# Kernel optimization log

Hardware: AMD Instinct MI355X
Metric: run time of the kernel (lower is better)

The kernel has to match this reference:

```python
import jax, jax.numpy as jnp
import numpy as np
from functools import partial

N_QUBITS = 8
DEPTH = 2
INPUT_DIM = 128
HIDDEN_DIM = N_QUBITS  # required: hx = o * tanh(cx) elementwise
DIM = 2 ** N_QUBITS

# Z expectation matrix: ZMAT[k, i] = +1/-1 depending on bit of basis state k at wire i
# (wire 0 is the most-significant qubit, PennyLane convention)
_bits = ((np.arange(DIM)[:, None] >> (N_QUBITS - 1 - np.arange(N_QUBITS)[None, :])) & 1)
ZMAT = jnp.asarray(1.0 - 2.0 * _bits, dtype=jnp.float32)  # [2**n, n]


def _apply_1q(state, G, wire):
    """Apply 2x2 gate G ([2,2] shared or [B,2,2] batched) on `wire`."""
    B = state.shape[0]
    left, right = 2 ** wire, 2 ** (N_QUBITS - wire - 1)
    s = state.reshape(B, left, 2, right)
    if G.ndim == 2:
        s = jnp.einsum('ij,bljr->blir', G, s)
    else:
        s = jnp.einsum('bij,bljr->blir', G, s)
    return s.reshape(B, DIM)


def _apply_cnot(state, wire):
    """CNOT with control=wire, target=wire+1 (adjacent)."""
    B = state.shape[0]
    left, right = 2 ** wire, 2 ** (N_QUBITS - wire - 2)
    s = state.reshape(B, left, 2, 2, right)
    s = jnp.concatenate([s[:, :, :1], s[:, :, 1:, ::-1]], axis=2)
    return s.reshape(B, DIM)


def quantum_gate(angles, params):
    """angles: [B, n] RX rotation angles; params: [depth, n] RY angles.
    Returns [B, n] PauliZ expectations (exact statevector simulation)."""
    B = angles.shape[0]
    state = jnp.zeros((B, DIM), dtype=jnp.complex64).at[:, 0].set(1.0)
    # RX encoding layer (batched angles)
    c = jnp.cos(angles / 2).astype(jnp.complex64)
    s = (-1j) * jnp.sin(angles / 2).astype(jnp.complex64)
    for i in range(N_QUBITS):
        G = jnp.stack([jnp.stack([c[:, i], s[:, i]], -1),
                       jnp.stack([s[:, i], c[:, i]], -1)], -2)  # [B,2,2]
        state = _apply_1q(state, G, i)
    # variational layers: RY (shared params) + CNOT chain
    cp = jnp.cos(params / 2).astype(jnp.complex64)
    sp = jnp.sin(params / 2).astype(jnp.complex64)
    for d in range(DEPTH):
        for i in range(N_QUBITS):
            G = jnp.array([[1.0, 0.0], [0.0, 1.0]], jnp.complex64)
            G = jnp.stack([jnp.stack([cp[d, i], -sp[d, i]]),
                           jnp.stack([sp[d, i], cp[d, i]])])  # [2,2]
            state = _apply_1q(state, G, i)
        for i in range(N_QUBITS - 1):
            state = _apply_cnot(state, i)
    probs = (state.real ** 2 + state.imag ** 2)  # [B, 2**n]
    return probs @ ZMAT  # [B, n]


def setup_inputs() -> dict:
    key = jax.random.key(0)
    ks = jax.random.split(key, 13)
    T, B = 256, 1024
    cat = INPUT_DIM + HIDDEN_DIM
    lin_scale = 1.0 / np.sqrt(cat)
    d = {'inputs': jax.random.normal(ks[0], (T, B, INPUT_DIM), jnp.float32)}
    for idx, g in enumerate(['f', 'i', 'g', 'o']):
        d[f'W{g}'] = jax.random.uniform(ks[1 + 3 * idx], (N_QUBITS, cat), jnp.float32, -lin_scale, lin_scale)
        d[f'b{g}'] = jax.random.uniform(ks[2 + 3 * idx], (N_QUBITS,), jnp.float32, -lin_scale, lin_scale)
        d[f'P{g}'] = jax.random.normal(ks[3 + 3 * idx], (DEPTH, N_QUBITS), jnp.float32)
    return d


def reference(inputs, Wf, bf, Pf, Wi, bi, Pi, Wg, bg, Pg, Wo, bo, Po):
    T, B, _ = inputs.shape
    h0 = jnp.zeros((B, HIDDEN_DIM), inputs.dtype)
    c0 = jnp.zeros((B, HIDDEN_DIM), inputs.dtype)

    def step(carry, x):
        hx, cx = carry
        comb = jnp.concatenate([x, hx], axis=1)  # [B, input+hidden]
        f = jax.nn.sigmoid(quantum_gate(comb @ Wf.T + bf, Pf))
        i = jax.nn.sigmoid(quantum_gate(comb @ Wi.T + bi, Pi))
        g = jnp.tanh(quantum_gate(comb @ Wg.T + bg, Pg))
        o = jax.nn.sigmoid(quantum_gate(comb @ Wo.T + bo, Po))
        cx = f * cx + i * g
        hx = o * jnp.tanh(cx)
        return (hx, cx), hx

    (hx, cx), outputs = jax.lax.scan(step, (h0, c0), inputs)
    return outputs, (hx, cx)
```

## Files before the change

### kernel.cpp

```cpp
#include <hip/hip_runtime.h>
#include <math.h>

#define TS 256
#define BB 1024
#define NQ 8
#define INDIM 128
#define CATDIM 136
#define INV2PI 0.15915494309189535f
#define LOG2E  1.4426950408889634f
#define CHUNK 32

typedef float v2f __attribute__((ext_vector_type(2)));

__device__ __forceinline__ float dpp_xor1(float v) {
    return __int_as_float(__builtin_amdgcn_mov_dpp(__float_as_int(v), 0xB1, 0xF, 0xF, true));
}
__device__ __forceinline__ float dpp_xor2(float v) {
    return __int_as_float(__builtin_amdgcn_mov_dpp(__float_as_int(v), 0x4E, 0xF, 0xF, true));
}
__device__ __forceinline__ float dpp_xor8(float v) {
    return __int_as_float(__builtin_amdgcn_mov_dpp(__float_as_int(v), 0x128, 0xF, 0xF, true));
}
__device__ __forceinline__ float swz4(float v)  {
    return __int_as_float(__builtin_amdgcn_ds_swizzle(__float_as_int(v), 0x101F));
}
__device__ __forceinline__ float swz16(float v) {
    return __int_as_float(__builtin_amdgcn_ds_swizzle(__float_as_int(v), 0x401F));
}
__device__ __forceinline__ float swz20(float v) {
    return __int_as_float(__builtin_amdgcn_ds_swizzle(__float_as_int(v), 0x501F));
}
__device__ __forceinline__ float hw_sin(float x) { float r; asm("v_sin_f32 %0, %1" : "=v"(r) : "v"(x)); return r; }
__device__ __forceinline__ float hw_cos(float x) { float r; asm("v_cos_f32 %0, %1" : "=v"(r) : "v"(x)); return r; }
__device__ __forceinline__ float hw_exp(float x) { float r; asm("v_exp_f32 %0, %1" : "=v"(r) : "v"(x)); return r; }
__device__ __forceinline__ float hw_rcp(float x) { float r; asm("v_rcp_f32 %0, %1" : "=v"(r) : "v"(x)); return r; }
__device__ __forceinline__ v2f mk2(float x, float y) { v2f r; r.x = x; r.y = y; return r; }
__device__ __forceinline__ v2f pk_fma(v2f a, v2f b, v2f c) {
    v2f d; asm("v_pk_fma_f32 %0, %1, %2, %3" : "=v"(d) : "v"(a), "v"(b), "v"(c)); return d;
}

__launch_bounds__(128, 1)
__global__ void qlstm_pc(const float* __restrict__ x,
    const float* __restrict__ Wf, const float* __restrict__ bf, const float* __restrict__ Pf,
    const float* __restrict__ Wi, const float* __restrict__ bi, const float* __restrict__ Pi,
    const float* __restrict__ Wg, const float* __restrict__ bg, const float* __restrict__ Pg,
    const float* __restrict__ Wo, const float* __restrict__ bo, const float* __restrict__ Po,
    float* __restrict__ out, float* __restrict__ hst, float* __restrict__ cst)
{
    const int tid = threadIdx.x;
    const int wv = tid >> 6;
    const int lane = tid & 63;
    const int b = blockIdx.x;

    __shared__ float xp[TS * 32];

    const float* Wlist[4] = { Wf, Wi, Wg, Wo };
    const float* blist[4] = { bf, bi, bg, bo };
    const float* Plist[4] = { Pf, Pi, Pg, Po };

    const int l0 = lane & 1, l1 = (lane >> 1) & 1, l3 = (lane >> 3) & 1;
    const int q = 4 * l0 + 2 * l1 + l3;
    const int g = ((lane >> 2) & 1) | ((lane >> 3) & 2);

    float Chw[8], nSw[8], hsp0[8], cp0c[8];
    v2f whq[4];
    float sel[8];
    float kl = 0.f, Aa = 0.f, Bb = 0.f;
    if (wv == 1) {
        const float* P = Plist[g];
        #pragma unroll
        for (int w = 0; w < 8; ++w) {
            float s1, c1, s0, c0;
            __sincosf(P[8 + w], &s1, &c1);
            __sincosf(P[w], &s0, &c0);
            Chw[w] = 0.5f * c1;
            nSw[w] = -s1;
            hsp0[w] = 0.5f * s0;
            cp0c[w] = c0;
        }
        const float* Wq = Wlist[g] + q * CATDIM + INDIM;
        #pragma unroll
        for (int p2 = 0; p2 < 4; ++p2)
            whq[p2] = mk2(INV2PI * Wq[q ^ (2 * p2)], INV2PI * Wq[q ^ (2 * p2 + 1)]);
        kl = ((g == 2) ? 2.f : -1.f) * LOG2E;
        Aa = (g == 2) ? 1.f : 0.f;
        Bb = (g == 2) ? -1.f : 1.f;
        #pragma unroll
        for (int i = 0; i < 8; ++i) sel[i] = (q == i) ? kl : 0.f;
    }

    float s0h = 0.f, s1h = 0.f, s2h = 0.f, s3h = 0.f;
    float s4h = 0.f, s5h = 0.f, s6h = 0.f, s7h = 0.f;
    float c_own = 0.f, hv = 0.f;
    const bool emit = (wv == 1) && ((lane & 0x34) == 0);
    float* optr = out + (size_t)b * NQ + q;

    const int pq = lane >> 3;
    const int kg = lane & 7;

    auto fill_chunk = [&](int base) {
        float4 wfrag[4][4];
        float bias_w[4];
        #pragma unroll
        for (int g4 = 0; g4 < 4; ++g4) {
            const float* Wr = Wlist[g4] + pq * CATDIM + kg * 16;
            #pragma unroll
            for (int c4 = 0; c4 < 4; ++c4) {
                float4 v = *(const float4*)(Wr + c4 * 4);
                v.x *= INV2PI; v.y *= INV2PI; v.z *= INV2PI; v.w *= INV2PI;
                wfrag[g4][c4] = v;
            }
            bias_w[g4] = blist[g4][pq] * INV2PI;
        }
        for (int tt = 0; tt < CHUNK; ++tt) {
            const int t = base + tt;
            const float* xr = x + ((size_t)t * BB + b) * INDIM + kg * 16;
            float4 x0 = *(const float4*)(xr);
            float4 x1 = *(const float4*)(xr + 4);
            float4 x2 = *(const float4*)(xr + 8);
            float4 x3 = *(const float4*)(xr + 12);
            #pragma unroll
            for (int g4 = 0; g4 < 4; ++g4) {
                float p =
                    x0.x*wfrag[g4][0].x + x0.y*wfrag[g4][0].y + x0.z*wfrag[g4][0].z + x0.w*wfrag[g4][0].w +
                    x1.x*wfrag[g4][1].x + x1.y*wfrag[g4][1].y + x1.z*wfrag[g4][1].z + x1.w*wfrag[g4][1].w +
                    x2.x*wfrag[g4][2].x + x2.y*wfrag[g4][2].y + x2.z*wfrag[g4][2].z + x2.w*wfrag[g4][2].w +
                    x3.x*wfrag[g4][3].x + x3.y*wfrag[g4][3].y + x3.z*wfrag[g4][3].z + x3.w*wfrag[g4][3].w;
                p += dpp_xor1(p);
                p += dpp_xor2(p);
                p += __shfl_xor(p, 4, 64);
                if (kg == 0) xp[t * 32 + g4 * 8 + pq] = p + bias_w[g4];
            }
        }
    };

    if (wv == 0) fill_chunk(0);
    __syncthreads();

    for (int k = 0; k < TS / CHUNK; ++k) {
        if (wv == 0) {
            if (k + 1 < TS / CHUNK) fill_chunk((k + 1) * CHUNK);
        } else {
            const int tbase = k * CHUNK;
            for (int tt = 0; tt < CHUNK; ++tt) {
                const int t = tbase + tt;
                float xb = xp[t * 32 + g * 8 + q];
                v2f hacc = pk_fma(mk2(s0h, s1h), whq[0], mk2(xb, 0.f));
                hacc = pk_fma(mk2(s2h, s3h), whq[1], hacc);
                hacc = pk_fma(mk2(s4h, s5h), whq[2], hacc);
                hacc = pk_fma(mk2(s6h, s7h), whq[3], hacc);
                float ang = hacc.x + hacc.y;

                float sa_own = hw_sin(ang);
                float ca_own = hw_cos(ang);

                float sa_0, sa_1, ca_0, ca_1;
                {
                    float p = dpp_xor1(sa_own);
                    sa_0 = l0 ? p : sa_own;  sa_1 = l0 ? sa_own : p;
                    p = dpp_xor1(ca_own);
                    ca_0 = l0 ? p : ca_own;  ca_1 = l0 ? ca_own : p;
                }
                float sa00, sa01, sa10, sa11, ca00, ca01, ca10, ca11;
                {
                    float p0 = dpp_xor2(sa_0), p1 = dpp_xor2(sa_1);
                    sa00 = l1 ? p0 : sa_0;  sa01 = l1 ? sa_0 : p0;
                    sa10 = l1 ? p1 : sa_1;  sa11 = l1 ? sa_1 : p1;
                    p0 = dpp_xor2(ca_0); p1 = dpp_xor2(ca_1);
                    ca00 = l1 ? p0 : ca_0;  ca01 = l1 ? ca_0 : p0;
                    ca10 = l1 ? p1 : ca_1;  ca11 = l1 ? ca_1 : p1;
                }
                float saw[8], caw[8];
                {
                    float p;
                    p = dpp_xor8(sa00); saw[0] = l3 ? p : sa00; saw[1] = l3 ? sa00 : p;
                    p = dpp_xor8(sa01); saw[2] = l3 ? p : sa01; saw[3] = l3 ? sa01 : p;
                    p = dpp_xor8(sa10); saw[4] = l3 ? p : sa10; saw[5] = l3 ? sa10 : p;
                    p = dpp_xor8(sa11); saw[6] = l3 ? p : sa11; saw[7] = l3 ? sa11 : p;
                    p = dpp_xor8(ca00); caw[0] = l3 ? p : ca00; caw[1] = l3 ? ca00 : p;
                    p = dpp_xor8(ca01); caw[2] = l3 ? p : ca01; caw[3] = l3 ? ca01 : p;
                    p = dpp_xor8(ca10); caw[4] = l3 ? p : ca10; caw[5] = l3 ? ca10 : p;
                    p = dpp_xor8(ca11); caw[6] = l3 ? p : ca11; caw[7] = l3 ? ca11 : p;
                }

                float kE = 0.f;
                float d0, d1, zr, zi;
                {
                    float AmB = cp0c[0] * caw[0];
                    d0 = Chw[0] * (1.f + AmB);
                    d1 = -(Chw[0] * (1.f - AmB));
                    zr = nSw[0] * (hsp0[0] * caw[0]);
                    zi = nSw[0] * (-0.5f * saw[0]);
                }
                #pragma unroll
                for (int w = 1; w < 8; ++w) {
                    float gr = hsp0[w] * caw[w];
                    float gi = -0.5f * saw[w];
                    float AmB = cp0c[w] * caw[w];
                    float sum = d0 + d1, dif = d0 - d1;
                    float p = gr * zr, qv = gi * zi;
                    float Ew = fmaf(4.f, p, sum);
                    kE = fmaf(sel[w - 1], Ew, kE);
                    float ad = AmB * dif;
                    float e1 = sum + ad, e3 = sum - ad;
                    float e2 = p - qv, e4 = p + qv;
                    float T0 = fmaf(4.f, e2, e1);
                    float T1 = fmaf(4.f, e4, e3);
                    float f1 = fmaf(gr, sum, zr);
                    float f3 = fmaf(AmB, zi, gi * dif);
                    d0 = Chw[w] * T0;
                    d1 = -(Chw[w] * T1);
                    zr = nSw[w] * f1;
                    zi = nSw[w] * f3;
                }
                {
                    float E7 = (d0 + d1) + 2.f * zr;
                    kE = fmaf(sel[7], E7, kE);
                }

                float y = hw_exp(kE);
                float a = fmaf(Aa, y, Bb) * hw_rcp(y + 1.f);

                float b4 = swz4(a);
                float b16 = swz16(a);
                float b20 = swz20(a);
                bool g1b = (g & 2) != 0;
                bool g0b = (g & 1) != 0;
                float e0 = g1b ? b16 : a;
                float e1s = g1b ? b20 : b4;
                float e2s = g1b ? a : b16;
                float e3s = g1b ? b4 : b20;
                float fv = g0b ? e1s : e0;
                float iv = g0b ? e0 : e1s;
                float gv = g0b ? e3s : e2s;
                float ov = g0b ? e2s : e3s;

                c_own = fmaf(fv, c_own, iv * gv);
                float e2c = hw_exp(c_own * (2.f * LOG2E));
                hv = ov * ((e2c - 1.f) * hw_rcp(e2c + 1.f));

                if (emit) *optr = hv;
                optr += (size_t)BB * NQ;

                s0h = hv;
                s4h = dpp_xor1(s0h);
                s2h = dpp_xor2(s0h);
                s6h = dpp_xor2(s4h);
                s1h = dpp_xor8(s0h);
                s5h = dpp_xor8(s4h);
                s3h = dpp_xor8(s2h);
                s7h = dpp_xor8(s6h);
            }
        }
        __syncthreads();
    }

    if (emit) {
        hst[b * NQ + q] = hv;
        cst[b * NQ + q] = c_own;
    }
}

extern "C" void kernel_launch(void* const* d_in, const int* in_sizes, int n_in,
                              void* d_out, int out_size, void* d_ws, size_t ws_size,
                              hipStream_t stream) {
    const float* x  = (const float*)d_in[0];
    const float* Wf = (const float*)d_in[1];
    const float* bf = (const float*)d_in[2];
    const float* Pf = (const float*)d_in[3];
    const float* Wi = (const float*)d_in[4];
    const float* bi = (const float*)d_in[5];
    const float* Pi = (const float*)d_in[6];
    const float* Wg = (const float*)d_in[7];
    const float* bg = (const float*)d_in[8];
    const float* Pg = (const float*)d_in[9];
    const float* Wo = (const float*)d_in[10];
    const float* bo = (const float*)d_in[11];
    const float* Po = (const float*)d_in[12];

    float* out = (float*)d_out;
    float* hst = out + (size_t)TS * BB * NQ;
    float* cst = hst + (size_t)BB * NQ;

    qlstm_pc<<<BB, 128, 0, stream>>>(x, Wf, bf, Pf, Wi, bi, Pi,
                                     Wg, bg, Pg, Wo, bo, Po,
                                     out, hst, cst);
}
```

Baseline: 238.9 us.

## Process four batch elements per block with two interleaved recurrences per lane

Each block now handles four batch elements instead of one, and the grid shrinks by four. The compute wave uses all 64 lanes, two groups of 32, each running two independent LSTM recurrences interleaved through a macro so the serial dependency chain gains instruction-level parallelism. The producer wave now computes input projections for all four elements into a larger shared buffer. The next-step input value is also prefetched from shared memory one step ahead. The risk is less parallelism across SIMDs, since there are fewer blocks per CU, plus a producer wave with four times the work per chunk.

```diff
diff --git a/kernel.cpp b/kernel.cpp
--- a/kernel.cpp
+++ b/kernel.cpp
@@ -39,8 +39,105 @@
     v2f d; asm("v_pk_fma_f32 %0, %1, %2, %3" : "=v"(d) : "v"(a), "v"(b), "v"(c)); return d;
 }
 
+#define STEP_EL(xbX, s0hX, s1hX, s2hX, s3hX, s4hX, s5hX, s6hX, s7hX, c_ownX, hvX) \
+    {                                                                             \
+        v2f hacc = pk_fma(mk2(s0hX, s1hX), whq[0], mk2(xbX, 0.f));                \
+        hacc = pk_fma(mk2(s2hX, s3hX), whq[1], hacc);                             \
+        hacc = pk_fma(mk2(s4hX, s5hX), whq[2], hacc);                             \
+        hacc = pk_fma(mk2(s6hX, s7hX), whq[3], hacc);                             \
+        float ang = hacc.x + hacc.y;                                              \
+        float sa_own = hw_sin(ang);                                               \
+        float ca_own = hw_cos(ang);                                               \
+        float sa_0, sa_1, ca_0, ca_1;                                             \
+        {                                                                         \
+            float p = dpp_xor1(sa_own);                                           \
+            sa_0 = l0 ? p : sa_own;  sa_1 = l0 ? sa_own : p;                      \
+            p = dpp_xor1(ca_own);                                                 \
+            ca_0 = l0 ? p : ca_own;  ca_1 = l0 ? ca_own : p;                      \
+        }                                                                         \
+        float sa00, sa01, sa10, sa11, ca00, ca01, ca10, ca11;                     \
+        {                                                                         \
+            float p0 = dpp_xor2(sa_0), p1 = dpp_xor2(sa_1);                       \
+            sa00 = l1 ? p0 : sa_0;  sa01 = l1 ? sa_0 : p0;                        \
+            sa10 = l1 ? p1 : sa_1;  sa11 = l1 ? sa_1 : p1;                        \
+            p0 = dpp_xor2(ca_0); p1 = dpp_xor2(ca_1);                             \
+            ca00 = l1 ? p0 : ca_0;  ca01 = l1 ? ca_0 : p0;                        \
+            ca10 = l1 ? p1 : ca_1;  ca11 = l1 ? ca_1 : p1;                        \
+        }                                                                         \
+        float saw[8], caw[8];                                                     \
+        {                                                                         \
+            float p;                                                              \
+            p = dpp_xor8(sa00); saw[0] = l3 ? p : sa00; saw[1] = l3 ? sa00 : p;   \
+            p = dpp_xor8(sa01); saw[2] = l3 ? p : sa01; saw[3] = l3 ? sa01 : p;   \
+            p = dpp_xor8(sa10); saw[4] = l3 ? p : sa10; saw[5] = l3 ? sa10 : p;   \
+            p = dpp_xor8(sa11); saw[6] = l3 ? p : sa11; saw[7] = l3 ? sa11 : p;   \
+            p = dpp_xor8(ca00); caw[0] = l3 ? p : ca00; caw[1] = l3 ? ca00 : p;   \
+            p = dpp_xor8(ca01); caw[2] = l3 ? p : ca01; caw[3] = l3 ? ca01 : p;   \
+            p = dpp_xor8(ca10); caw[4] = l3 ? p : ca10; caw[5] = l3 ? ca10 : p;   \
+            p = dpp_xor8(ca11); caw[6] = l3 ? p : ca11; caw[7] = l3 ? ca11 : p;   \
+        }                                                                         \
+        float kE = 0.f;                                                           \
+        float d0, d1, zr, zi;                                                     \
+        {                                                                         \
+            float AmB = cp0c[0] * caw[0];                                         \
+            d0 = Chw[0] * (1.f + AmB);                                            \
+            d1 = -(Chw[0] * (1.f - AmB));                                         \
+            zr = nSw[0] * (hsp0[0] * caw[0]);                                     \
+            zi = nSw[0] * (-0.5f * saw[0]);                                       \
+        }                                                                         \
+        _Pragma("unroll")                                                         \
+        for (int w = 1; w < 8; ++w) {                                             \
+            float gr = hsp0[w] * caw[w];                                          \
+            float gi = -0.5f * saw[w];                                            \
+            float AmB = cp0c[w] * caw[w];                                         \
+            float sum = d0 + d1, dif = d0 - d1;                                   \
+            float p = gr * zr, qv = gi * zi;                                      \
+            float Ew = fmaf(4.f, p, sum);                                         \
+            kE = fmaf(sel[w - 1], Ew, kE);                                        \
+            float ad = AmB * dif;                                                 \
+            float e1 = sum + ad, e3 = sum - ad;                                   \
+            float e2 = p - qv, e4 = p + qv;                                       \
+            float T0 = fmaf(4.f, e2, e1);                                         \
+            float T1 = fmaf(4.f, e4, e3);                                         \
+            float f1 = fmaf(gr, sum, zr);                                         \
+            float f3 = fmaf(AmB, zi, gi * dif);                                   \
+            d0 = Chw[w] * T0;                                                     \
+            d1 = -(Chw[w] * T1);                                                  \
+            zr = nSw[w] * f1;                                                     \
+            zi = nSw[w] * f3;                                                     \
+        }                                                                         \
+        {                                                                         \
+            float E7 = (d0 + d1) + 2.f * zr;                                      \
+            kE = fmaf(sel[7], E7, kE);                                            \
+        }                                                                         \
+        float y = hw_exp(kE);                                                     \
+        float a = fmaf(Aa, y, Bb) * hw_rcp(y + 1.f);                              \
+        float b4 = swz4(a);                                                       \
+        float b16 = swz16(a);                                                     \
+        float b20 = swz20(a);                                                     \
+        float e0 = g1b ? b16 : a;                                                 \
+        float e1s = g1b ? b20 : b4;                                               \
+        float e2s = g1b ? a : b16;                                                \
+        float e3s = g1b ? b4 : b20;                                               \
+        float fv = g0b ? e1s : e0;                                                \
+        float iv = g0b ? e0 : e1s;                                                \
+        float gv = g0b ? e3s : e2s;                                               \
+        float ov = g0b ? e2s : e3s;                                               \
+        c_ownX = fmaf(fv, c_ownX, iv * gv);                                       \
+        float e2c = hw_exp(c_ownX * (2.f * LOG2E));                               \
+        hvX = ov * ((e2c - 1.f) * hw_rcp(e2c + 1.f));                             \
+        s0hX = hvX;                                                               \
+        s4hX = dpp_xor1(s0hX);                                                    \
+        s2hX = dpp_xor2(s0hX);                                                    \
+        s6hX = dpp_xor2(s4hX);                                                    \
+        s1hX = dpp_xor8(s0hX);                                                    \
+        s5hX = dpp_xor8(s4hX);                                                    \
+        s3hX = dpp_xor8(s2hX);                                                    \
+        s7hX = dpp_xor8(s6hX);                                                    \
+    }
+
 __launch_bounds__(128, 1)
-__global__ void qlstm_pc(const float* __restrict__ x,
+__global__ void qlstm_pc4(const float* __restrict__ x,
     const float* __restrict__ Wf, const float* __restrict__ bf, const float* __restrict__ Pf,
     const float* __restrict__ Wi, const float* __restrict__ bi, const float* __restrict__ Pi,
     const float* __restrict__ Wg, const float* __restrict__ bg, const float* __restrict__ Pg,
@@ -50,55 +147,16 @@
     const int tid = threadIdx.x;
     const int wv = tid >> 6;
     const int lane = tid & 63;
-    const int b = blockIdx.x;
-
-    __shared__ float xp[TS * 32];
+
+    __shared__ float xp[4 * TS * 32];
 
     const float* Wlist[4] = { Wf, Wi, Wg, Wo };
     const float* blist[4] = { bf, bi, bg, bo };
     const float* Plist[4] = { Pf, Pi, Pg, Po };
 
-    const int l0 = lane & 1, l1 = (lane >> 1) & 1, l3 = (lane >> 3) & 1;
-    const int q = 4 * l0 + 2 * l1 + l3;
-    const int g = ((lane >> 2) & 1) | ((lane >> 3) & 2);
-
-    float Chw[8], nSw[8], hsp0[8], cp0c[8];
-    v2f whq[4];
-    float sel[8];
-    float kl = 0.f, Aa = 0.f, Bb = 0.f;
-    if (wv == 1) {
-        const float* P = Plist[g];
-        #pragma unroll
-        for (int w = 0; w < 8; ++w) {
-            float s1, c1, s0, c0;
-            __sincosf(P[8 + w], &s1, &c1);
-            __sincosf(P[w], &s0, &c0);
-            Chw[w] = 0.5f * c1;
-            nSw[w] = -s1;
-            hsp0[w] = 0.5f * s0;
-            cp0c[w] = c0;
-        }
-        const float* Wq = Wlist[g] + q * CATDIM + INDIM;
-        #pragma unroll
-        for (int p2 = 0; p2 < 4; ++p2)
-            whq[p2] = mk2(INV2PI * Wq[q ^ (2 * p2)], INV2PI * Wq[q ^ (2 * p2 + 1)]);
-        kl = ((g == 2) ? 2.f : -1.f) * LOG2E;
-        Aa = (g == 2) ? 1.f : 0.f;
-        Bb = (g == 2) ? -1.f : 1.f;
-        #pragma unroll
-        for (int i = 0; i < 8; ++i) sel[i] = (q == i) ? kl : 0.f;
-    }
-
-    float s0h = 0.f, s1h = 0.f, s2h = 0.f, s3h = 0.f;
-    float s4h = 0.f, s5h = 0.f, s6h = 0.f, s7h = 0.f;
-    float c_own = 0.f, hv = 0.f;
-    const bool emit = (wv == 1) && ((lane & 0x34) == 0);
-    float* optr = out + (size_t)b * NQ + q;
-
-    const int pq = lane >> 3;
-    const int kg = lane & 7;
-
-    auto fill_chunk = [&](int base) {
+    if (wv == 0) {
+        const int pq = lane >> 3;
+        const int kg = lane & 7;
         float4 wfrag[4][4];
         float bias_w[4];
         #pragma unroll
@@ -112,152 +170,119 @@
             }
             bias_w[g4] = blist[g4][pq] * INV2PI;
         }
-        for (int tt = 0; tt < CHUNK; ++tt) {
-            const int t = base + tt;
-            const float* xr = x + ((size_t)t * BB + b) * INDIM + kg * 16;
-            float4 x0 = *(const float4*)(xr);
-            float4 x1 = *(const float4*)(xr + 4);
-            float4 x2 = *(const float4*)(xr + 8);
-            float4 x3 = *(const float4*)(xr + 12);
+
+        auto fill_chunk = [&](int base) {
+            #pragma unroll 1
+            for (int el = 0; el < 4; ++el) {
+                const int b = blockIdx.x * 4 + el;
+                for (int tt = 0; tt < CHUNK; ++tt) {
+                    const int t = base + tt;
+                    const float* xr = x + ((size_t)t * BB + b) * INDIM + kg * 16;
+                    float4 x0 = *(const float4*)(xr);
+                    float4 x1 = *(const float4*)(xr + 4);
+                    float4 x2 = *(const float4*)(xr + 8);
+                    float4 x3 = *(const float4*)(xr + 12);
+                    #pragma unroll
+                    for (int g4 = 0; g4 < 4; ++g4) {
+                        float p =
+                            x0.x*wfrag[g4][0].x + x0.y*wfrag[g4][0].y + x0.z*wfrag[g4][0].z + x0.w*wfrag[g4][0].w +
+                            x1.x*wfrag[g4][1].x + x1.y*wfrag[g4][1].y + x1.z*wfrag[g4][1].z + x1.w*wfrag[g4][1].w +
+                            x2.x*wfrag[g4][2].x + x2.y*wfrag[g4][2].y + x2.z*wfrag[g4][2].z + x2.w*wfrag[g4][2].w +
+                            x3.x*wfrag[g4][3].x + x3.y*wfrag[g4][3].y + x3.z*wfrag[g4][3].z + x3.w*wfrag[g4][3].w;
+                        p += dpp_xor1(p);
+                        p += dpp_xor2(p);
+                        p += __shfl_xor(p, 4, 64);
+                        if (kg == 0) xp[(el * TS + t) * 32 + g4 * 8 + pq] = p + bias_w[g4];
+                    }
+                }
+            }
+        };
+
+        fill_chunk(0);
+        __syncthreads();
+        for (int k = 0; k < TS / CHUNK; ++k) {
+            if (k + 1 < TS / CHUNK) fill_chunk((k + 1) * CHUNK);
+            __syncthreads();
+        }
+    } else {
+        const int l0 = lane & 1, l1 = (lane >> 1) & 1, l3 = (lane >> 3) & 1;
+        const int q = 4 * l0 + 2 * l1 + l3;
+        const int g = ((lane >> 2) & 1) | ((lane >> 3) & 2);
+        const int el2 = lane >> 5;
+        const int bA = blockIdx.x * 4 + el2 * 2;
+        const int bB = bA + 1;
+        const bool g1b = (g & 2) != 0;
+        const bool g0b = (g & 1) != 0;
+
+        const float* P = Plist[g];
+        float Chw[8], nSw[8], hsp0[8], cp0c[8];
+        #pragma unroll
+        for (int w = 0; w < 8; ++w) {
+            float s1, c1, s0, c0;
+            __sincosf(P[8 + w], &s1, &c1);
+            __sincosf(P[w], &s0, &c0);
+            Chw[w] = 0.5f * c1;
+            nSw[w] = -s1;
+            hsp0[w] = 0.5f * s0;
+            cp0c[w] = c0;
+        }
+        v2f whq[4];
+        {
+            const float* Wq = Wlist[g] + q * CATDIM + INDIM;
             #pragma unroll
-            for (int g4 = 0; g4 < 4; ++g4) {
-                float p =
-                    x0.x*wfrag[g4][0].x + x0.y*wfrag[g4][0].y + x0.z*wfrag[g4][0].z + x0.w*wfrag[g4][0].w +
-                    x1.x*wfrag[g4][1].x + x1.y*wfrag[g4][1].y + x1.z*wfrag[g4][1].z + x1.w*wfrag[g4][1].w +
-                    x2.x*wfrag[g4][2].x + x2.y*wfrag[g4][2].y + x2.z*wfrag[g4][2].z + x2.w*wfrag[g4][2].w +
-                    x3.x*wfrag[g4][3].x + x3.y*wfrag[g4][3].y + x3.z*wfrag[g4][3].z + x3.w*wfrag[g4][3].w;
-                p += dpp_xor1(p);
-                p += dpp_xor2(p);
-                p += __shfl_xor(p, 4, 64);
-                if (kg == 0) xp[t * 32 + g4 * 8 + pq] = p + bias_w[g4];
-            }
-        }
-    };
-
-    if (wv == 0) fill_chunk(0);
-    __syncthreads();
-
-    for (int k = 0; k < TS / CHUNK; ++k) {
-        if (wv == 0) {
-            if (k + 1 < TS / CHUNK) fill_chunk((k + 1) * CHUNK);
-        } else {
+            for (int p2 = 0; p2 < 4; ++p2)
+                whq[p2] = mk2(INV2PI * Wq[q ^ (2 * p2)], INV2PI * Wq[q ^ (2 * p2 + 1)]);
+        }
+        const float kl = ((g == 2) ? 2.f : -1.f) * LOG2E;
+        const float Aa = (g == 2) ? 1.f : 0.f;
+        const float Bb = (g == 2) ? -1.f : 1.f;
+        float sel[8];
+        #pragma unroll
+        for (int i = 0; i < 8; ++i) sel[i] = (q == i) ? kl : 0.f;
+
+        float s0hA = 0.f, s1hA = 0.f, s2hA = 0.f, s3hA = 0.f;
+        float s4hA = 0.f, s5hA = 0.f, s6hA = 0.f, s7hA = 0.f;
+        float s0hB = 0.f, s1hB = 0.f, s2hB = 0.f, s3hB = 0.f;
+        float s4hB = 0.f, s5hB = 0.f, s6hB = 0.f, s7hB = 0.f;
+        float c_ownA = 0.f, hvA = 0.f, c_ownB = 0.f, hvB = 0.f;
+
+        const bool emit = (lane & 0x14) == 0;
+        float* optrA = out + (size_t)bA * NQ + q;
+        float* optrB = out + (size_t)bB * NQ + q;
+        const int offA = (el2 * 2) * (TS * 32) + g * 8 + q;
+        const int offB = offA + TS * 32;
+
+        __syncthreads();
+        for (int k = 0; k < TS / CHUNK; ++k) {
             const int tbase = k * CHUNK;
+            float xbA = xp[offA + tbase * 32];
+            float xbB = xp[offB + tbase * 32];
             for (int tt = 0; tt < CHUNK; ++tt) {
                 const int t = tbase + tt;
-                float xb = xp[t * 32 + g * 8 + q];
-                v2f hacc = pk_fma(mk2(s0h, s1h), whq[0], mk2(xb, 0.f));
-                hacc = pk_fma(mk2(s2h, s3h), whq[1], hacc);
-                hacc = pk_fma(mk2(s4h, s5h), whq[2], hacc);
-                hacc = pk_fma(mk2(s6h, s7h), whq[3], hacc);
-                float ang = hacc.x + hacc.y;
-
-                float sa_own = hw_sin(ang);
-                float ca_own = hw_cos(ang);
-
-                float sa_0, sa_1, ca_0, ca_1;
-                {
-                    float p = dpp_xor1(sa_own);
-                    sa_0 = l0 ? p : sa_own;  sa_1 = l0 ? sa_own : p;
-                    p = dpp_xor1(ca_own);
-                    ca_0 = l0 ? p : ca_own;  ca_1 = l0 ? ca_own : p;
+                float nxA = xbA, nxB = xbB;
+                if (tt + 1 < CHUNK) {
+                    nxA = xp[offA + (t + 1) * 32];
+                    nxB = xp[offB + (t + 1) * 32];
                 }
-                float sa00, sa01, sa10, sa11, ca00, ca01, ca10, ca11;
-                {
-                    float p0 = dpp_xor2(sa_0), p1 = dpp_xor2(sa_1);
-                    sa00 = l1 ? p0 : sa_0;  sa01 = l1 ? sa_0 : p0;
-                    sa10 = l1 ? p1 : sa_1;  sa11 = l1 ? sa_1 : p1;
-                    p0 = dpp_xor2(ca_0); p1 = dpp_xor2(ca_1);
-                    ca00 = l1 ? p0 : ca_0;  ca01 = l1 ? ca_0 : p0;
-                    ca10 = l1 ? p1 : ca_1;  ca11 = l1 ? ca_1 : p1;
-                }
-                float saw[8], caw[8];
-                {
-                    float p;
-                    p = dpp_xor8(sa00); saw[0] = l3 ? p : sa00; saw[1] = l3 ? sa00 : p;
-                    p = dpp_xor8(sa01); saw[2] = l3 ? p : sa01; saw[3] = l3 ? sa01 : p;
-                    p = dpp_xor8(sa10); saw[4] = l3 ? p : sa10; saw[5] = l3 ? sa10 : p;
-                    p = dpp_xor8(sa11); saw[6] = l3 ? p : sa11; saw[7] = l3 ? sa11 : p;
-                    p = dpp_xor8(ca00); caw[0] = l3 ? p : ca00; caw[1] = l3 ? ca00 : p;
-                    p = dpp_xor8(ca01); caw[2] = l3 ? p : ca01; caw[3] = l3 ? ca01 : p;
-                    p = dpp_xor8(ca10); caw[4] = l3 ? p : ca10; caw[5] = l3 ? ca10 : p;
-                    p = dpp_xor8(ca11); caw[6] = l3 ? p : ca11; caw[7] = l3 ? ca11 : p;
-                }
-
-                float kE = 0.f;
-                float d0, d1, zr, zi;
-                {
-                    float AmB = cp0c[0] * caw[0];
-                    d0 = Chw[0] * (1.f + AmB);
-                    d1 = -(Chw[0] * (1.f - AmB));
-                    zr = nSw[0] * (hsp0[0] * caw[0]);
-                    zi = nSw[0] * (-0.5f * saw[0]);
-                }
-                #pragma unroll
-                for (int w = 1; w < 8; ++w) {
-                    float gr = hsp0[w] * caw[w];
-                    float gi = -0.5f * saw[w];
-                    float AmB = cp0c[w] * caw[w];
-                    float sum = d0 + d1, dif = d0 - d1;
-                    float p = gr * zr, qv = gi * zi;
-                    float Ew = fmaf(4.f, p, sum);
-                    kE = fmaf(sel[w - 1], Ew, kE);
-                    float ad = AmB * dif;
-                    float e1 = sum + ad, e3 = sum - ad;
-                    float e2 = p - qv, e4 = p + qv;
-                    float T0 = fmaf(4.f, e2, e1);
-                    float T1 = fmaf(4.f, e4, e3);
-                    float f1 = fmaf(gr, sum, zr);
-                    float f3 = fmaf(AmB, zi, gi * dif);
-                    d0 = Chw[w] * T0;
-                    d1 = -(Chw[w] * T1);
-                    zr = nSw[w] * f1;
-                    zi = nSw[w] * f3;
-                }
-                {
-                    float E7 = (d0 + d1) + 2.f * zr;
-                    kE = fmaf(sel[7], E7, kE);
-                }
-
-                float y = hw_exp(kE);
-                float a = fmaf(Aa, y, Bb) * hw_rcp(y + 1.f);
-
-                float b4 = swz4(a);
-                float b16 = swz16(a);
-                float b20 = swz20(a);
-                bool g1b = (g & 2) != 0;
-                bool g0b = (g & 1) != 0;
-                float e0 = g1b ? b16 : a;
-                float e1s = g1b ? b20 : b4;
-                float e2s = g1b ? a : b16;
-                float e3s = g1b ? b4 : b20;
-                float fv = g0b ? e1s : e0;
-                float iv = g0b ? e0 : e1s;
-                float gv = g0b ? e3s : e2s;
-                float ov = g0b ? e2s : e3s;
-
-                c_own = fmaf(fv, c_own, iv * gv);
-                float e2c = hw_exp(c_own * (2.f * LOG2E));
-                hv = ov * ((e2c - 1.f) * hw_rcp(e2c + 1.f));
-
-                if (emit) *optr = hv;
-                optr += (size_t)BB * NQ;
-
-                s0h = hv;
-                s4h = dpp_xor1(s0h);
-                s2h = dpp_xor2(s0h);
-                s6h = dpp_xor2(s4h);
-                s1h = dpp_xor8(s0h);
-                s5h = dpp_xor8(s4h);
-                s3h = dpp_xor8(s2h);
-                s7h = dpp_xor8(s6h);
+
+                STEP_EL(xbA, s0hA, s1hA, s2hA, s3hA, s4hA, s5hA, s6hA, s7hA, c_ownA, hvA)
+                STEP_EL(xbB, s0hB, s1hB, s2hB, s3hB, s4hB, s5hB, s6hB, s7hB, c_ownB, hvB)
+
+                if (emit) { *optrA = hvA; *optrB = hvB; }
+                optrA += (size_t)BB * NQ;
+                optrB += (size_t)BB * NQ;
+
+                xbA = nxA; xbB = nxB;
             }
-        }
-        __syncthreads();
-    }
-
-    if (emit) {
-        hst[b * NQ + q] = hv;
-        cst[b * NQ + q] = c_own;
+            __syncthreads();
+        }
+
+        if (emit) {
+            hst[bA * NQ + q] = hvA;
+            cst[bA * NQ + q] = c_ownA;
+            hst[bB * NQ + q] = hvB;
+            cst[bB * NQ + q] = c_ownB;
+        }
     }
 }
 
@@ -282,7 +307,7 @@
     float* hst = out + (size_t)TS * BB * NQ;
     float* cst = hst + (size_t)BB * NQ;
 
-    qlstm_pc<<<BB, 128, 0, stream>>>(x, Wf, bf, Pf, Wi, bi, Pi,
-                                     Wg, bg, Pg, Wo, bo, Po,
-                                     out, hst, cst);
-}
+    qlstm_pc4<<<BB / 4, 128, 0, stream>>>(x, Wf, bf, Pf, Wi, bi, Pi,
+                                          Wg, bg, Pg, Wo, bo, Po,
+                                          out, hst, cst);
+}
```

Result: slower. 648.8 us (+171.6%).
